# Performance work log

Measured on AMD Instinct MI355X. Metric: run time of the kernel, lower is better.

## Reference

```python
import jax, jax.numpy as jnp
import numpy as np
import math

DIM = 256
HEADS = 8
D_K = DIM // HEADS
B, N = 16, 128


def _linear_params(key, dim):
    k1, k2 = jax.random.split(key)
    bound = 1.0 / math.sqrt(dim)
    W = jax.random.uniform(k1, (dim, dim), jnp.float32, -bound, bound)
    b = jax.random.uniform(k2, (dim,), jnp.float32, -bound, bound)
    return W, b


def setup_inputs() -> dict:
    key = jax.random.key(0)
    keys = jax.random.split(key, 8)
    node = jax.random.normal(keys[0], (B, N, DIM), jnp.float32)
    edge = jax.random.normal(keys[1], (B, N, N, DIM), jnp.float32)
    Wq, bq = _linear_params(keys[2], DIM)
    Wk, bk = _linear_params(keys[3], DIM)
    Wv, bv = _linear_params(keys[4], DIM)
    We, be = _linear_params(keys[5], DIM)
    Woe, boe = _linear_params(keys[6], DIM)
    Won, bon = _linear_params(keys[7], DIM)
    return {"node": node, "edge": edge,
            "Wq": Wq, "bq": bq, "Wk": Wk, "bk": bk, "Wv": Wv, "bv": bv,
            "We": We, "be": be, "Woe": Woe, "boe": boe, "Won": Won, "bon": bon}


def reference(node, edge, Wq, bq, Wk, bk, Wv, bv, We, be, Woe, boe, Won, bon):
    b, n, c = node.shape
    heads, d_k = HEADS, c // HEADS
    inv_sqrt_dk = 1.0 / math.sqrt(d_k)
    # projections (torch Linear: x @ W.T + b)
    q = (node @ Wq.T + bq).reshape(b, n, heads, d_k)   # [b,n,h,d]
    k = (node @ Wk.T + bk).reshape(b, n, heads, d_k)
    v = (node @ Wv.T + bv).reshape(b, n, heads, d_k)
    e = (edge @ We.T + be).reshape(b, n, n, heads, d_k)  # [b,n,n,h,d]
    # elementwise pairwise attention scores, edge-gated
    attn = q[:, :, None] * k[:, None]                   # [b,n,n,h,d]
    attn = attn * inv_sqrt_dk
    attn = attn * (e + 1.0) * e
    # edge output: project flattened head dim
    edge_out = attn.reshape(b, n, n, c) @ Woe.T + boe   # [b,n,n,c]
    # softmax over key-node axis (dim=2), per-channel
    a = jax.nn.softmax(attn, axis=2)                    # [b,n,n,h,d]
    # weighted sum over key nodes
    node_agg = jnp.einsum('bijhd,bjhd->bihd', a, v).reshape(b, n, c)
    node_out = node_agg @ Won.T + bon                   # [b,n,c]
    return node_out, edge_out
```

## Files before the change

### kernel.cpp

```cpp
#include <hip/hip_runtime.h>

#define SCALE 0.17677669529663687f

typedef __attribute__((ext_vector_type(8))) __bf16 bf16x8;
typedef __attribute__((ext_vector_type(8))) unsigned short u16x8;
typedef __attribute__((ext_vector_type(4))) float f32x4;

__device__ inline float bf2f(unsigned short s) {
    union { unsigned int u; float f; } x; x.u = ((unsigned int)s) << 16; return x.f;
}
__device__ inline unsigned short f2bf(float f) {
    union { float f; unsigned int u; } x; x.f = f;
    return (unsigned short)((x.u + 0x7fffu + ((x.u >> 16) & 1u)) >> 16);
}
__device__ inline u16x8 cvt8(float4 a, float4 b) {
    u16x8 p;
    p[0] = f2bf(a.x); p[1] = f2bf(a.y); p[2] = f2bf(a.z); p[3] = f2bf(a.w);
    p[4] = f2bf(b.x); p[5] = f2bf(b.y); p[6] = f2bf(b.z); p[7] = f2bf(b.w);
    return p;
}
__device__ inline int offT(int row, int c8) { return row * 64 + ((c8 ^ row) & 7) * 8; }
__device__ inline int offAttn(int j, int c8) { return j * 256 + (((c8) & 24) | ((c8 ^ j) & 7)) * 8; }

__global__ void __launch_bounds__(256) prep_kernel(
    const float* __restrict__ We, const float* __restrict__ Woe,
    unsigned short* __restrict__ pWe, unsigned short* __restrict__ pWoe)
{
    const int id = blockIdx.x * 256 + threadIdx.x;
    const float* W = (id & 8192) ? Woe : We;
    unsigned short* P = (id & 8192) ? pWoe : pWe;
    const int rem = id & 8191;
    const int kt = rem >> 11, chunk = rem & 2047, row = chunk >> 3, c8 = chunk & 7;
    const float* s = W + row * 256 + kt * 64 + c8 * 8;
    *(u16x8*)(P + kt * 16384 + offT(row, c8)) = cvt8(*(const float4*)s, *(const float4*)(s + 4));
}

__global__ void __launch_bounds__(256) qkv_kernel(
    const float* __restrict__ node,
    const float* __restrict__ Wq, const float* __restrict__ bq,
    const float* __restrict__ Wk, const float* __restrict__ bk,
    const float* __restrict__ Wv, const float* __restrict__ bv,
    float* __restrict__ qs, float* __restrict__ kf, float* __restrict__ vf)
{
    __shared__ __align__(16) unsigned short As[128 * 64], Bs[128 * 64];
    const int wsel = blockIdx.y >> 1;
    const int halfn = (blockIdx.y & 1) * 128;
    const float* W    = wsel == 0 ? Wq : (wsel == 1 ? Wk : Wv);
    const float* bias = wsel == 0 ? bq : (wsel == 1 ? bk : bv);
    float*       out  = wsel == 0 ? qs : (wsel == 1 ? kf : vf);
    const float scl = wsel == 0 ? SCALE : 1.0f;
    const int tid = threadIdx.x, lane = tid & 63, wid = tid >> 6;
    const int wM = (wid >> 1) * 64, wN = (wid & 1) * 64;
    const int fr = lane & 15, quad = lane >> 4;
    const size_t M0 = (size_t)blockIdx.x * 128;

    f32x4 acc[4][4];
#pragma unroll
    for (int i = 0; i < 4; ++i)
#pragma unroll
        for (int j = 0; j < 4; ++j) acc[i][j] = (f32x4){0.f, 0.f, 0.f, 0.f};

    for (int kt = 0; kt < 4; ++kt) {
        __syncthreads();
#pragma unroll
        for (int i = 0; i < 4; ++i) {
            const int c = tid + i * 256, row = c >> 3, c8 = c & 7;
            const float* sa = node + (M0 + row) * 256 + kt * 64 + c8 * 8;
            const float* sb = W + (size_t)(halfn + row) * 256 + kt * 64 + c8 * 8;
            *(u16x8*)(As + offT(row, c8)) = cvt8(*(const float4*)sa, *(const float4*)(sa + 4));
            *(u16x8*)(Bs + offT(row, c8)) = cvt8(*(const float4*)sb, *(const float4*)(sb + 4));
        }
        __syncthreads();
#pragma unroll
        for (int ks = 0; ks < 2; ++ks) {
            bf16x8 af[4], bb[4];
#pragma unroll
            for (int mb = 0; mb < 4; ++mb) {
                const int row = wM + mb * 16 + fr;
                af[mb] = *(const bf16x8*)(As + offT(row, ks * 4 + quad));
            }
#pragma unroll
            for (int nb = 0; nb < 4; ++nb) {
                const int row = wN + nb * 16 + fr;
                bb[nb] = *(const bf16x8*)(Bs + offT(row, ks * 4 + quad));
            }
#pragma unroll
            for (int mb = 0; mb < 4; ++mb)
#pragma unroll
                for (int nb = 0; nb < 4; ++nb)
                    acc[mb][nb] = __builtin_amdgcn_mfma_f32_16x16x32_bf16(af[mb], bb[nb], acc[mb][nb], 0, 0, 0);
        }
    }
#pragma unroll
    for (int nb = 0; nb < 4; ++nb) {
        const int gc = halfn + wN + nb * 16 + fr;
        const float bv_ = bias[gc];
#pragma unroll
        for (int mb = 0; mb < 4; ++mb)
#pragma unroll
            for (int r = 0; r < 4; ++r) {
                const int j = wM + mb * 16 + quad * 4 + r;
                out[(M0 + j) * 256 + gc] = (acc[mb][nb][r] + bv_) * scl;
            }
    }
}

__global__ void __launch_bounds__(256) won_kernel(
    const float* __restrict__ agg, const float* __restrict__ Won,
    const float* __restrict__ bon, float* __restrict__ out_node)
{
    __shared__ __align__(16) unsigned short As[128 * 64], Bs[128 * 64];
    const int halfn = blockIdx.y * 128;
    const int tid = threadIdx.x, lane = tid & 63, wid = tid >> 6;
    const int wM = (wid >> 1) * 64, wN = (wid & 1) * 64;
    const int fr = lane & 15, quad = lane >> 4;
    const size_t M0 = (size_t)blockIdx.x * 128;

    f32x4 acc[4][4];
#pragma unroll
    for (int i = 0; i < 4; ++i)
#pragma unroll
        for (int j = 0; j < 4; ++j) acc[i][j] = (f32x4){0.f, 0.f, 0.f, 0.f};

    for (int kt = 0; kt < 4; ++kt) {
        __syncthreads();
#pragma unroll
        for (int i = 0; i < 4; ++i) {
            const int c = tid + i * 256, row = c >> 3, c8 = c & 7;
            const float* sa = agg + (M0 + row) * 256 + kt * 64 + c8 * 8;
            const float* sb = Won + (size_t)(halfn + row) * 256 + kt * 64 + c8 * 8;
            *(u16x8*)(As + offT(row, c8)) = cvt8(*(const float4*)sa, *(const float4*)(sa + 4));
            *(u16x8*)(Bs + offT(row, c8)) = cvt8(*(const float4*)sb, *(const float4*)(sb + 4));
        }
        __syncthreads();
#pragma unroll
        for (int ks = 0; ks < 2; ++ks) {
            bf16x8 af[4], bb[4];
#pragma unroll
            for (int mb = 0; mb < 4; ++mb)
                af[mb] = *(const bf16x8*)(As + offT(wM + mb * 16 + fr, ks * 4 + quad));
#pragma unroll
            for (int nb = 0; nb < 4; ++nb)
                bb[nb] = *(const bf16x8*)(Bs + offT(wN + nb * 16 + fr, ks * 4 + quad));
#pragma unroll
            for (int mb = 0; mb < 4; ++mb)
#pragma unroll
                for (int nb = 0; nb < 4; ++nb)
                    acc[mb][nb] = __builtin_amdgcn_mfma_f32_16x16x32_bf16(af[mb], bb[nb], acc[mb][nb], 0, 0, 0);
        }
    }
#pragma unroll
    for (int nb = 0; nb < 4; ++nb) {
        const int gc = halfn + wN + nb * 16 + fr;
        const float bv_ = bon[gc];
#pragma unroll
        for (int mb = 0; mb < 4; ++mb)
#pragma unroll
            for (int r = 0; r < 4; ++r) {
                const int j = wM + mb * 16 + quad * 4 + r;
                out_node[(M0 + j) * 256 + gc] = acc[mb][nb][r] + bv_;
            }
    }
}

__global__ void __launch_bounds__(512, 4) fused_kernel(
    const float* __restrict__ edge,
    const unsigned short* __restrict__ pWe,  const float* __restrict__ be,
    const unsigned short* __restrict__ pWoe, const float* __restrict__ boe,
    const float* __restrict__ qs, const float* __restrict__ kf, const float* __restrict__ vf,
    float* __restrict__ aggout, float* __restrict__ out_edge)
{
    extern __shared__ __align__(16) char smem[];
    unsigned short* attn_s = (unsigned short*)smem;
    float*          sred   = (float*)(smem + 65536);

    const int mtile = blockIdx.x;
    const int tid = threadIdx.x, lane = tid & 63, wid = tid >> 6;
    const int wM = (wid >> 2) * 64;
    const int wN = (wid & 3) * 64;
    const int fr = lane & 15, quad = lane >> 4;
    const size_t rowA0 = (size_t)mtile * 128;
    const int b128 = (mtile >> 7) * 128;

    {
        const int c8 = tid & 31, r0 = tid >> 5;
        float4 ea[8], eb[8];
#pragma unroll
        for (int i = 0; i < 8; ++i) {
            const float* s = edge + (rowA0 + i * 16 + r0) * 256 + c8 * 8;
            ea[i] = *(const float4*)s; eb[i] = *(const float4*)(s + 4);
        }
#pragma unroll
        for (int i = 0; i < 8; ++i)
            *(u16x8*)(attn_s + offAttn(i * 16 + r0, c8)) = cvt8(ea[i], eb[i]);
    }
    __syncthreads();

    f32x4 acc[4][4];
#pragma unroll
    for (int i = 0; i < 4; ++i)
#pragma unroll
        for (int j = 0; j < 4; ++j) acc[i][j] = (f32x4){0.f, 0.f, 0.f, 0.f};

#pragma unroll
    for (int kt = 0; kt < 4; ++kt) {
        const unsigned short* BW = pWe + kt * 16384;
#pragma unroll
        for (int ks = 0; ks < 2; ++ks) {
            bf16x8 af[4], bb[4];
#pragma unroll
            for (int mb = 0; mb < 4; ++mb)
                af[mb] = *(const bf16x8*)(attn_s + offAttn(wM + mb * 16 + fr, kt * 8 + ks * 4 + quad));
#pragma unroll
            for (int nb = 0; nb < 4; ++nb)
                bb[nb] = *(const bf16x8*)(BW + offT(wN + nb * 16 + fr, ks * 4 + quad));
#pragma unroll
            for (int mb = 0; mb < 4; ++mb)
#pragma unroll
                for (int nb = 0; nb < 4; ++nb)
                    acc[mb][nb] = __builtin_amdgcn_mfma_f32_16x16x32_bf16(af[mb], bb[nb], acc[mb][nb], 0, 0, 0);
        }
    }
    __syncthreads();

    {
        const float* qrow = qs + (size_t)mtile * 256;
#pragma unroll
        for (int nb = 0; nb < 4; ++nb) {
            const int gc = wN + nb * 16 + fr;
            const float qv = qrow[gc], bev = be[gc];
            const int c8 = gc >> 3, cl = gc & 7;
#pragma unroll
            for (int mb = 0; mb < 4; ++mb)
#pragma unroll
                for (int r = 0; r < 4; ++r) {
                    const int j = wM + mb * 16 + quad * 4 + r;
                    const float e = acc[mb][nb][r] + bev;
                    const float kv = kf[(size_t)(b128 + j) * 256 + gc];
                    attn_s[offAttn(j, c8) + cl] = f2bf(qv * kv * (e + 1.0f) * e);
                }
        }
    }
    __syncthreads();

    f32x4 acc2[4][4];
#pragma unroll
    for (int i = 0; i < 4; ++i)
#pragma unroll
        for (int j = 0; j < 4; ++j) acc2[i][j] = (f32x4){0.f, 0.f, 0.f, 0.f};

#pragma unroll
    for (int kt = 0; kt < 4; ++kt) {
        const unsigned short* BW = pWoe + kt * 16384;
#pragma unroll
        for (int ks = 0; ks < 2; ++ks) {
            bf16x8 af[4], bb[4];
#pragma unroll
            for (int mb = 0; mb < 4; ++mb) {
                const int row = wM + mb * 16 + fr;
                af[mb] = *(const bf16x8*)(attn_s + offAttn(row, kt * 8 + ks * 4 + quad));
            }
#pragma unroll
            for (int nb = 0; nb < 4; ++nb)
                bb[nb] = *(const bf16x8*)(BW + offT(wN + nb * 16 + fr, ks * 4 + quad));
#pragma unroll
            for (int mb = 0; mb < 4; ++mb)
#pragma unroll
                for (int nb = 0; nb < 4; ++nb)
                    acc2[mb][nb] = __builtin_amdgcn_mfma_f32_16x16x32_bf16(af[mb], bb[nb], acc2[mb][nb], 0, 0, 0);
        }
    }
#pragma unroll
    for (int nb = 0; nb < 4; ++nb) {
        const int gc = wN + nb * 16 + fr;
        const float bo = boe[gc];
#pragma unroll
        for (int mb = 0; mb < 4; ++mb)
#pragma unroll
            for (int r = 0; r < 4; ++r) {
                const int j = wM + mb * 16 + quad * 4 + r;
                out_edge[((size_t)mtile * 128 + j) * 256 + gc] = acc2[mb][nb][r] + bo;
            }
    }

    const int c = tid & 255, hlf = tid >> 8;
    const int cc8 = c >> 3, ccl = c & 7;
    float m = -1e30f;
#pragma unroll 8
    for (int j2 = 0; j2 < 64; ++j2) {
        const int j = hlf * 64 + j2;
        m = fmaxf(m, bf2f(attn_s[offAttn(j, cc8) + ccl]));
    }
    sred[hlf * 256 + c] = m;
    __syncthreads();
    const float M = fmaxf(sred[c], sred[256 + c]);
    float l = 0.f, av = 0.f;
#pragma unroll 4
    for (int j2 = 0; j2 < 64; ++j2) {
        const int j = hlf * 64 + j2;
        const float w = __expf(bf2f(attn_s[offAttn(j, cc8) + ccl]) - M);
        l += w;
        av += w * vf[(size_t)(b128 + j) * 256 + c];
    }
    float* sl = sred + 512; float* sav = sred + 1024;
    sl[hlf * 256 + c] = l; sav[hlf * 256 + c] = av;
    __syncthreads();
    if (tid < 256) {
        const float L = sl[c] + sl[256 + c], AV = sav[c] + sav[256 + c];
        aggout[(size_t)mtile * 256 + c] = AV / L;
    }
}

extern "C" void kernel_launch(void* const* d_in, const int* in_sizes, int n_in,
                              void* d_out, int out_size, void* d_ws, size_t ws_size,
                              hipStream_t stream) {
    const float* node = (const float*)d_in[0];
    const float* edge = (const float*)d_in[1];
    const float* Wq   = (const float*)d_in[2];
    const float* bq   = (const float*)d_in[3];
    const float* Wk   = (const float*)d_in[4];
    const float* bk   = (const float*)d_in[5];
    const float* Wv   = (const float*)d_in[6];
    const float* bv   = (const float*)d_in[7];
    const float* We   = (const float*)d_in[8];
    const float* be   = (const float*)d_in[9];
    const float* Woe  = (const float*)d_in[10];
    const float* boe  = (const float*)d_in[11];
    const float* Won  = (const float*)d_in[12];
    const float* bon  = (const float*)d_in[13];

    float* out_node = (float*)d_out;
    float* out_edge = out_node + (size_t)2048 * 256;

    char* ws = (char*)d_ws;
    unsigned short* pWe  = (unsigned short*)ws;
    unsigned short* pWoe = (unsigned short*)(ws + 131072);
    float* qs = (float*)(ws + 262144);
    float* kf = qs + (size_t)2048 * 256;
    float* vf = kf + (size_t)2048 * 256;
    float* agg = qs;

    static const int lds_bytes = 71680;
    hipFuncSetAttribute((const void*)fused_kernel,
                        hipFuncAttributeMaxDynamicSharedMemorySize, lds_bytes);

    hipLaunchKernelGGL(prep_kernel, dim3(64), dim3(256), 0, stream, We, Woe, pWe, pWoe);
    hipLaunchKernelGGL(qkv_kernel, dim3(16, 6), dim3(256), 0, stream,
                       node, Wq, bq, Wk, bk, Wv, bv, qs, kf, vf);
    hipLaunchKernelGGL(fused_kernel, dim3(2048), dim3(512), lds_bytes, stream,
                       edge, pWe, be, pWoe, boe, qs, kf, vf, agg, out_edge);
    hipLaunchKernelGGL(won_kernel, dim3(16, 2), dim3(256), 0, stream,
                       agg, Won, bon, out_node);
}
```

Baseline: 641.3 us.

## Split fused edge kernel into two row halves with online softmax to cut LDS

The fused edge kernel now handles its 128 key rows in two 64-row halves. Each half streams the edge K-slices through a small 8KB staging buffer, prefetching the next slice into registers, instead of loading the whole 128x256 tile up front. Softmax statistics are combined across halves with an online (rescaled) max/sum. LDS use drops from about 70KB to 40KB and the launch bound hint is raised, aiming for more resident blocks and overlap of global loads with MFMA, at the cost of more barriers and smaller per-wave MFMA tiles.

```diff
diff --git a/kernel.cpp b/kernel.cpp
--- a/kernel.cpp
+++ b/kernel.cpp
@@ -163,7 +163,7 @@
     }
 }
 
-__global__ void __launch_bounds__(512, 4) fused_kernel(
+__global__ void __launch_bounds__(512, 6) fused_kernel(
     const float* __restrict__ edge,
     const unsigned short* __restrict__ pWe,  const float* __restrict__ be,
     const unsigned short* __restrict__ pWoe, const float* __restrict__ boe,
@@ -172,142 +172,151 @@
 {
     extern __shared__ __align__(16) char smem[];
     unsigned short* attn_s = (unsigned short*)smem;
-    float*          sred   = (float*)(smem + 65536);
+    unsigned short* As     = (unsigned short*)(smem + 32768);
+    float*          sred   = (float*)(smem + 32768);
 
     const int mtile = blockIdx.x;
     const int tid = threadIdx.x, lane = tid & 63, wid = tid >> 6;
-    const int wM = (wid >> 2) * 64;
+    const int wM = (wid >> 2) * 32;
     const int wN = (wid & 3) * 64;
     const int fr = lane & 15, quad = lane >> 4;
     const size_t rowA0 = (size_t)mtile * 128;
     const int b128 = (mtile >> 7) * 128;
 
+    const int srow = tid >> 3, sc8 = tid & 7;
+    float4 pa, pb;
     {
-        const int c8 = tid & 31, r0 = tid >> 5;
-        float4 ea[8], eb[8];
-#pragma unroll
-        for (int i = 0; i < 8; ++i) {
-            const float* s = edge + (rowA0 + i * 16 + r0) * 256 + c8 * 8;
-            ea[i] = *(const float4*)s; eb[i] = *(const float4*)(s + 4);
-        }
-#pragma unroll
-        for (int i = 0; i < 8; ++i)
-            *(u16x8*)(attn_s + offAttn(i * 16 + r0, c8)) = cvt8(ea[i], eb[i]);
-    }
-    __syncthreads();
-
-    f32x4 acc[4][4];
-#pragma unroll
-    for (int i = 0; i < 4; ++i)
-#pragma unroll
-        for (int j = 0; j < 4; ++j) acc[i][j] = (f32x4){0.f, 0.f, 0.f, 0.f};
-
-#pragma unroll
-    for (int kt = 0; kt < 4; ++kt) {
-        const unsigned short* BW = pWe + kt * 16384;
-#pragma unroll
-        for (int ks = 0; ks < 2; ++ks) {
-            bf16x8 af[4], bb[4];
-#pragma unroll
-            for (int mb = 0; mb < 4; ++mb)
-                af[mb] = *(const bf16x8*)(attn_s + offAttn(wM + mb * 16 + fr, kt * 8 + ks * 4 + quad));
-#pragma unroll
-            for (int nb = 0; nb < 4; ++nb)
-                bb[nb] = *(const bf16x8*)(BW + offT(wN + nb * 16 + fr, ks * 4 + quad));
-#pragma unroll
-            for (int mb = 0; mb < 4; ++mb)
+        const float* s = edge + (rowA0 + srow) * 256 + sc8 * 8;
+        pa = *(const float4*)s; pb = *(const float4*)(s + 4);
+    }
+
+    const int c = tid & 255, sub = tid >> 8;
+    const int cc8 = c >> 3, ccl = c & 7;
+    float m_t = -1e30f, l_t = 0.f, av_t = 0.f;
+
+    const float* qrow = qs + (size_t)mtile * 256;
+
+    for (int h = 0; h < 2; ++h) {
+        f32x4 acc[2][4];
+#pragma unroll
+        for (int i = 0; i < 2; ++i)
+#pragma unroll
+            for (int j = 0; j < 4; ++j) acc[i][j] = (f32x4){0.f, 0.f, 0.f, 0.f};
+
+        for (int kt = 0; kt < 4; ++kt) {
+            __syncthreads();
+            *(u16x8*)(As + offT(srow, sc8)) = cvt8(pa, pb);
+            __syncthreads();
+            if (kt < 3 || h == 0) {
+                const int nh = (kt < 3) ? h : 1, nkt = (kt + 1) & 3;
+                const float* s = edge + (rowA0 + nh * 64 + srow) * 256 + nkt * 64 + sc8 * 8;
+                pa = *(const float4*)s; pb = *(const float4*)(s + 4);
+            }
+            const unsigned short* BW = pWe + kt * 16384;
+#pragma unroll
+            for (int ks = 0; ks < 2; ++ks) {
+                bf16x8 af[2], bb[4];
+#pragma unroll
+                for (int mb = 0; mb < 2; ++mb)
+                    af[mb] = *(const bf16x8*)(As + offT(wM + mb * 16 + fr, ks * 4 + quad));
 #pragma unroll
                 for (int nb = 0; nb < 4; ++nb)
-                    acc[mb][nb] = __builtin_amdgcn_mfma_f32_16x16x32_bf16(af[mb], bb[nb], acc[mb][nb], 0, 0, 0);
-        }
-    }
-    __syncthreads();
-
-    {
-        const float* qrow = qs + (size_t)mtile * 256;
+                    bb[nb] = *(const bf16x8*)(BW + offT(wN + nb * 16 + fr, ks * 4 + quad));
+#pragma unroll
+                for (int mb = 0; mb < 2; ++mb)
+#pragma unroll
+                    for (int nb = 0; nb < 4; ++nb)
+                        acc[mb][nb] = __builtin_amdgcn_mfma_f32_16x16x32_bf16(af[mb], bb[nb], acc[mb][nb], 0, 0, 0);
+            }
+        }
+
+        {
+#pragma unroll
+            for (int nb = 0; nb < 4; ++nb) {
+                const int gc = wN + nb * 16 + fr;
+                const float qv = qrow[gc], bev = be[gc];
+                const int c8 = gc >> 3, cl = gc & 7;
+#pragma unroll
+                for (int mb = 0; mb < 2; ++mb)
+#pragma unroll
+                    for (int r = 0; r < 4; ++r) {
+                        const int j = wM + mb * 16 + quad * 4 + r;
+                        const float e = acc[mb][nb][r] + bev;
+                        const float kv = kf[(size_t)(b128 + h * 64 + j) * 256 + gc];
+                        attn_s[offAttn(j, c8) + cl] = f2bf(qv * kv * (e + 1.0f) * e);
+                    }
+            }
+        }
+        __syncthreads();
+
+        f32x4 acc2[2][4];
+#pragma unroll
+        for (int i = 0; i < 2; ++i)
+#pragma unroll
+            for (int j = 0; j < 4; ++j) acc2[i][j] = (f32x4){0.f, 0.f, 0.f, 0.f};
+
+#pragma unroll
+        for (int kt = 0; kt < 4; ++kt) {
+            const unsigned short* BW = pWoe + kt * 16384;
+#pragma unroll
+            for (int ks = 0; ks < 2; ++ks) {
+                bf16x8 af[2], bb[4];
+#pragma unroll
+                for (int mb = 0; mb < 2; ++mb)
+                    af[mb] = *(const bf16x8*)(attn_s + offAttn(wM + mb * 16 + fr, kt * 8 + ks * 4 + quad));
+#pragma unroll
+                for (int nb = 0; nb < 4; ++nb)
+                    bb[nb] = *(const bf16x8*)(BW + offT(wN + nb * 16 + fr, ks * 4 + quad));
+#pragma unroll
+                for (int mb = 0; mb < 2; ++mb)
+#pragma unroll
+                    for (int nb = 0; nb < 4; ++nb)
+                        acc2[mb][nb] = __builtin_amdgcn_mfma_f32_16x16x32_bf16(af[mb], bb[nb], acc2[mb][nb], 0, 0, 0);
+            }
+        }
 #pragma unroll
         for (int nb = 0; nb < 4; ++nb) {
             const int gc = wN + nb * 16 + fr;
-            const float qv = qrow[gc], bev = be[gc];
-            const int c8 = gc >> 3, cl = gc & 7;
-#pragma unroll
-            for (int mb = 0; mb < 4; ++mb)
+            const float bo = boe[gc];
+#pragma unroll
+            for (int mb = 0; mb < 2; ++mb)
 #pragma unroll
                 for (int r = 0; r < 4; ++r) {
                     const int j = wM + mb * 16 + quad * 4 + r;
-                    const float e = acc[mb][nb][r] + bev;
-                    const float kv = kf[(size_t)(b128 + j) * 256 + gc];
-                    attn_s[offAttn(j, c8) + cl] = f2bf(qv * kv * (e + 1.0f) * e);
+                    out_edge[((size_t)mtile * 128 + h * 64 + j) * 256 + gc] = acc2[mb][nb][r] + bo;
                 }
         }
-    }
-    __syncthreads();
-
-    f32x4 acc2[4][4];
-#pragma unroll
-    for (int i = 0; i < 4; ++i)
-#pragma unroll
-        for (int j = 0; j < 4; ++j) acc2[i][j] = (f32x4){0.f, 0.f, 0.f, 0.f};
-
-#pragma unroll
-    for (int kt = 0; kt < 4; ++kt) {
-        const unsigned short* BW = pWoe + kt * 16384;
-#pragma unroll
-        for (int ks = 0; ks < 2; ++ks) {
-            bf16x8 af[4], bb[4];
-#pragma unroll
-            for (int mb = 0; mb < 4; ++mb) {
-                const int row = wM + mb * 16 + fr;
-                af[mb] = *(const bf16x8*)(attn_s + offAttn(row, kt * 8 + ks * 4 + quad));
-            }
-#pragma unroll
-            for (int nb = 0; nb < 4; ++nb)
-                bb[nb] = *(const bf16x8*)(BW + offT(wN + nb * 16 + fr, ks * 4 + quad));
-#pragma unroll
-            for (int mb = 0; mb < 4; ++mb)
-#pragma unroll
-                for (int nb = 0; nb < 4; ++nb)
-                    acc2[mb][nb] = __builtin_amdgcn_mfma_f32_16x16x32_bf16(af[mb], bb[nb], acc2[mb][nb], 0, 0, 0);
-        }
-    }
-#pragma unroll
-    for (int nb = 0; nb < 4; ++nb) {
-        const int gc = wN + nb * 16 + fr;
-        const float bo = boe[gc];
-#pragma unroll
-        for (int mb = 0; mb < 4; ++mb)
-#pragma unroll
-            for (int r = 0; r < 4; ++r) {
-                const int j = wM + mb * 16 + quad * 4 + r;
-                out_edge[((size_t)mtile * 128 + j) * 256 + gc] = acc2[mb][nb][r] + bo;
-            }
-    }
-
-    const int c = tid & 255, hlf = tid >> 8;
-    const int cc8 = c >> 3, ccl = c & 7;
-    float m = -1e30f;
+
+        {
+            float mh = -1e30f;
 #pragma unroll 8
-    for (int j2 = 0; j2 < 64; ++j2) {
-        const int j = hlf * 64 + j2;
-        m = fmaxf(m, bf2f(attn_s[offAttn(j, cc8) + ccl]));
-    }
-    sred[hlf * 256 + c] = m;
-    __syncthreads();
-    const float M = fmaxf(sred[c], sred[256 + c]);
-    float l = 0.f, av = 0.f;
+            for (int j2 = 0; j2 < 32; ++j2)
+                mh = fmaxf(mh, bf2f(attn_s[offAttn(sub * 32 + j2, cc8) + ccl]));
+            const float newm = fmaxf(m_t, mh);
+            const float scale = __expf(m_t - newm);
+            l_t *= scale; av_t *= scale; m_t = newm;
 #pragma unroll 4
-    for (int j2 = 0; j2 < 64; ++j2) {
-        const int j = hlf * 64 + j2;
-        const float w = __expf(bf2f(attn_s[offAttn(j, cc8) + ccl]) - M);
-        l += w;
-        av += w * vf[(size_t)(b128 + j) * 256 + c];
-    }
-    float* sl = sred + 512; float* sav = sred + 1024;
-    sl[hlf * 256 + c] = l; sav[hlf * 256 + c] = av;
+            for (int j2 = 0; j2 < 32; ++j2) {
+                const int j = sub * 32 + j2;
+                const float w = __expf(bf2f(attn_s[offAttn(j, cc8) + ccl]) - m_t);
+                l_t += w;
+                av_t += w * vf[(size_t)(b128 + h * 64 + j) * 256 + c];
+            }
+        }
+    }
+
+    float* sm  = sred;
+    float* sl  = sred + 512;
+    float* sav = sred + 1024;
+    sm[tid] = m_t; sl[tid] = l_t; sav[tid] = av_t;
     __syncthreads();
     if (tid < 256) {
-        const float L = sl[c] + sl[256 + c], AV = sav[c] + sav[256 + c];
-        aggout[(size_t)mtile * 256 + c] = AV / L;
+        const float m0 = sm[tid], m1 = sm[tid + 256];
+        const float M = fmaxf(m0, m1);
+        const float s0 = __expf(m0 - M), s1 = __expf(m1 - M);
+        const float L  = sl[tid] * s0 + sl[tid + 256] * s1;
+        const float AV = sav[tid] * s0 + sav[tid + 256] * s1;
+        aggout[(size_t)mtile * 256 + tid] = AV / L;
     }
 }
 
@@ -340,7 +349,7 @@
     float* vf = kf + (size_t)2048 * 256;
     float* agg = qs;
 
-    static const int lds_bytes = 71680;
+    static const int lds_bytes = 40960;
     hipFuncSetAttribute((const void*)fused_kernel,
                         hipFuncAttributeMaxDynamicSharedMemorySize, lds_bytes);
 
```

Measured after the change: 1.564 ms. 2.44x slower.
